# Kernel tuning notes

Measured on AMD Instinct MI355X. Metric: run time of the kernel, lower is better.

## Reference

```python
import jax, jax.numpy as jnp
import numpy as np
from jax import lax

NUM_SAMPLES = 16
EPSILON = 1e-08
CHUNK = 1024  # tile size for the reverse NN search (matches torch batch_size)


def _cdist(a, b):
    # Euclidean distance matrix [Na, Nb] via gemm form, numerically floored for sqrt.
    d2 = (a * a).sum(-1)[:, None] + (b * b).sum(-1)[None, :] - 2.0 * (a @ b.T)
    return jnp.sqrt(jnp.maximum(d2, 1e-12))


def setup_inputs() -> dict:
    key = jax.random.key(0)
    k = jax.random.split(key, 6)
    N, F, M, G = 16384, 16384, 4096, 8192
    return {
        "original_vertices": jax.random.normal(k[0], (N, 3), dtype=jnp.float32),
        "original_faces": jax.random.randint(k[1], (F, 3), 0, N),
        "simplified_vertices": jax.random.normal(k[2], (M, 3), dtype=jnp.float32),
        "simplified_faces": jax.random.randint(k[3], (G, 3), 0, M),
        "face_probabilities": jax.random.uniform(k[4], (G,), dtype=jnp.float32),
        "r1": jax.random.uniform(k[5], (G, NUM_SAMPLES, 1), dtype=jnp.float32),
        "r2": jax.random.uniform(jax.random.fold_in(key, 7), (G, NUM_SAMPLES, 1), dtype=jnp.float32),
    }


def reference(original_vertices, original_faces, simplified_vertices,
              simplified_faces, face_probabilities, r1, r2):
    G = simplified_faces.shape[0]
    probs = face_probabilities[:G]  # pad/slice to num simplified faces (identity here)

    # ---- forward term: simplified barycenters -> nearest original barycenter ----
    orig_bary = original_vertices[original_faces].mean(axis=1)      # [F,3]
    simp_bary = simplified_vertices[simplified_faces].mean(axis=1)  # [G,3]
    min_d = _cdist(simp_bary, orig_bary).min(axis=1)                # [G]
    forward_term = (probs * min_d).sum() + 1e-4 * (1.0 - probs).sum()

    # ---- reverse term: sample points on simplified faces, NN to original verts ----
    sqrt_r1 = jnp.sqrt(r1)
    u = 1.0 - sqrt_r1
    v = sqrt_r1 * (1.0 - r2)
    w = sqrt_r1 * r2
    fv = simplified_vertices[simplified_faces]  # [G,3,3]
    pts = (u * fv[:, None, 0] + v * fv[:, None, 1] + w * fv[:, None, 2]).reshape(-1, 3)

    total = pts.shape[0]  # G * NUM_SAMPLES, divisible by CHUNK
    vsq = (original_vertices * original_vertices).sum(-1)  # [N]

    def chunk_min(p):  # p: [CHUNK, 3]
        d2 = (p * p).sum(-1)[:, None] + vsq[None, :] - 2.0 * (p @ original_vertices.T)
        return jnp.sqrt(jnp.maximum(d2, 1e-12)).min(axis=1)

    mins = lax.map(chunk_min, pts.reshape(total // CHUNK, CHUNK, 3)).reshape(-1)
    max_dist = mins.max() + EPSILON
    scaled = mins / max_dist * 0.1
    probs_exp = jnp.repeat(probs, NUM_SAMPLES)
    reverse_term = (probs_exp * scaled).sum()

    return forward_term + reverse_term
```

## Files before the change

kernel.cpp:

```cpp
#include <hip/hip_runtime.h>
#include <math.h>

constexpr int N_V  = 16384;
constexpr int N_F  = 16384;
constexpr int G_F  = 8192;
constexpr int NS   = 16;
constexpr int NPTS = G_F * NS;

constexpr int MB    = 2;
constexpr int TILES = 32;

typedef _Float16 half8 __attribute__((ext_vector_type(8)));
typedef float    f32x16 __attribute__((ext_vector_type(16)));

constexpr int F4_ACC   = 0;
constexpr int F4_SB    = 1;
constexpr int F4_PTS   = F4_SB + G_F;
constexpr int F4_PKV   = F4_PTS + NPTS;
constexpr int F4_PKO   = F4_PKV + 32768;
constexpr int F4_TOTAL = F4_PKO + 32768;
constexpr int WS_MINF  = F4_TOTAL * 4;
constexpr int WS_MINR  = WS_MINF + G_F;

__device__ __forceinline__ void mfma4(half8 a0, half8 a1, half8 cA, half8 cB,
                                      f32x16& d0A, f32x16& d0B,
                                      f32x16& d1A, f32x16& d1B) {
  asm("v_mfma_f32_32x32x16_f16 %0, %4, %6, 0\n\t"
      "v_mfma_f32_32x32x16_f16 %1, %4, %7, 0\n\t"
      "v_mfma_f32_32x32x16_f16 %2, %5, %6, 0\n\t"
      "v_mfma_f32_32x32x16_f16 %3, %5, %7, 0\n\t"
      "s_nop 7\n\t"
      "s_nop 7\n\t"
      "s_nop 7\n\t"
      "s_nop 7\n\t"
      "s_nop 7\n\t"
      "s_nop 7"
      : "=&v"(d0A), "=&v"(d0B), "=&v"(d1A), "=&v"(d1B)
      : "v"(a0), "v"(a1), "v"(cA), "v"(cB));
}

__device__ __forceinline__ void pack_target(float x, float y, float z, float sq,
                                            half8* __restrict__ pk, int tile, int n) {
  float ax = -2.0f*x, ay = -2.0f*y, az = -2.0f*z;
  _Float16 hx = (_Float16)ax, hy = (_Float16)ay, hz = (_Float16)az, hw = (_Float16)sq;
  _Float16 lx = (_Float16)(ax - (float)hx), ly = (_Float16)(ay - (float)hy);
  _Float16 lz = (_Float16)(az - (float)hz), lw = (_Float16)(sq - (float)hw);
  half8 h0; h0[0]=hx; h0[1]=hy; h0[2]=hz; h0[3]=hw; h0[4]=lx; h0[5]=ly; h0[6]=lz; h0[7]=lw;
  half8 h1; h1[0]=hx; h1[1]=hy; h1[2]=hz; h1[3]=hw;
  h1[4]=(_Float16)0.0f; h1[5]=(_Float16)0.0f; h1[6]=(_Float16)0.0f; h1[7]=(_Float16)0.0f;
  pk[(size_t)tile*64 + n]      = h0;
  pk[(size_t)tile*64 + 32 + n] = h1;
}

__global__ void k_prep(const float* __restrict__ ov, const int* __restrict__ of,
                       const float* __restrict__ sv, const int* __restrict__ sf,
                       const float* __restrict__ r1, const float* __restrict__ r2,
                       unsigned int* __restrict__ ws, float4* __restrict__ ws4) {
  int i = blockIdx.x * blockDim.x + threadIdx.x;
  if (i < 4) ws[i] = 0u;
  ws[WS_MINR + i] = 0x7f800000u;

  {
    int g = i >> 4;
    int a = sf[3*g], b = sf[3*g+1], c = sf[3*g+2];
    float sr = sqrtf(r1[i]);
    float u = 1.0f - sr;
    float v = sr * (1.0f - r2[i]);
    float w = sr * r2[i];
    float px = u*sv[3*a]   + v*sv[3*b]   + w*sv[3*c];
    float py = u*sv[3*a+1] + v*sv[3*b+1] + w*sv[3*c+1];
    float pz = u*sv[3*a+2] + v*sv[3*b+2] + w*sv[3*c+2];
    (ws4 + F4_PTS)[i] = make_float4(px, py, pz, fmaf(px, px, fmaf(py, py, pz*pz)));
  }
  if (i < G_F) {
    ws[WS_MINF + i] = 0x7f800000u;
    int a = sf[3*i], b = sf[3*i+1], c = sf[3*i+2];
    float x = (sv[3*a] + sv[3*b] + sv[3*c]) * (1.0f/3.0f);
    float y = (sv[3*a+1] + sv[3*b+1] + sv[3*c+1]) * (1.0f/3.0f);
    float z = (sv[3*a+2] + sv[3*b+2] + sv[3*c+2]) * (1.0f/3.0f);
    (ws4 + F4_SB)[i] = make_float4(x, y, z, fmaf(x, x, fmaf(y, y, z*z)));
  }
  if (i < N_V) {
    float x = ov[3*i], y = ov[3*i+1], z = ov[3*i+2];
    pack_target(x, y, z, fmaf(x, x, fmaf(y, y, z*z)),
                (half8*)(ws4 + F4_PKV), i >> 5, i & 31);
  }
  if (i < N_F) {
    int a = of[3*i], b = of[3*i+1], c = of[3*i+2];
    float x = (ov[3*a] + ov[3*b] + ov[3*c]) * (1.0f/3.0f);
    float y = (ov[3*a+1] + ov[3*b+1] + ov[3*c+1]) * (1.0f/3.0f);
    float z = (ov[3*a+2] + ov[3*b+2] + ov[3*c+2]) * (1.0f/3.0f);
    pack_target(x, y, z, fmaf(x, x, fmaf(y, y, z*z)),
                (half8*)(ws4 + F4_PKO), i >> 5, i & 31);
  }
}

__global__ __launch_bounds__(256, 3) void k_min(const float4* __restrict__ q4,
                                                const half8* __restrict__ pk,
                                                unsigned int* __restrict__ minU,
                                                int nchunks) {
  __shared__ half8 sB[TILES * 64];
  int lane  = threadIdx.x & 63;
  int wave  = threadIdx.x >> 6;
  int half_ = lane >> 5;
  int m     = lane & 31;
  int qbase = blockIdx.x * 256 + wave * (32 * MB);
  int tbase = blockIdx.y * nchunks * TILES;

  half8 afrag[MB];
  float psq[MB];
  #pragma unroll
  for (int mb = 0; mb < MB; ++mb) {
    float4 q = q4[qbase + mb*32 + m];
    psq[mb] = q.w;
    _Float16 hx = (_Float16)q.x, hy = (_Float16)q.y, hz = (_Float16)q.z;
    half8 a;
    if (half_ == 0) {
      a[0]=hx; a[1]=hy; a[2]=hz; a[3]=(_Float16)1.0f;
      a[4]=hx; a[5]=hy; a[6]=hz; a[7]=(_Float16)1.0f;
    } else {
      a[0]=(_Float16)(q.x-(float)hx); a[1]=(_Float16)(q.y-(float)hy);
      a[2]=(_Float16)(q.z-(float)hz); a[3]=(_Float16)0.0f;
      a[4]=(_Float16)0.0f; a[5]=(_Float16)0.0f; a[6]=(_Float16)0.0f; a[7]=(_Float16)0.0f;
    }
    afrag[mb] = a;
  }

  float inf = __uint_as_float(0x7f800000u);
  float rm[MB][16];
  #pragma unroll
  for (int mb = 0; mb < MB; ++mb)
    #pragma unroll
    for (int r = 0; r < 16; ++r) rm[mb][r] = inf;

  for (int ch = 0; ch < nchunks; ++ch) {
    int t0 = tbase + ch * TILES;
    if (ch > 0) __syncthreads();
    const half8* src = pk + (size_t)(t0 + wave) * 64 + lane;
    #pragma unroll
    for (int j = 0; j < TILES/4; ++j) {
      __builtin_amdgcn_global_load_lds(
          (const __attribute__((address_space(1))) unsigned int*)(src + (size_t)j*256),
          (__attribute__((address_space(3))) unsigned int*)&sB[(wave + 4*j) * 64],
          16, 0, 0);
    }
    __syncthreads();

    for (int t = 0; t < TILES; t += 2) {
      half8 cA = sB[t*64 + lane];
      half8 cB = sB[t*64 + 64 + lane];
      f32x16 dA, dB, eA, eB;
      mfma4(afrag[0], afrag[1], cA, cB, dA, dB, eA, eB);
      #pragma unroll
      for (int r = 0; r < 16; ++r)
        rm[0][r] = fminf(fminf(rm[0][r], dA[r]), dB[r]);
      #pragma unroll
      for (int r = 0; r < 16; ++r)
        rm[1][r] = fminf(fminf(rm[1][r], eA[r]), eB[r]);
    }
  }

  #pragma unroll
  for (int mb = 0; mb < MB; ++mb) {
    #pragma unroll
    for (int r = 0; r < 16; ++r) {
      float v = rm[mb][r];
      v = fminf(v, __shfl_xor(v, 1, 64));
      v = fminf(v, __shfl_xor(v, 2, 64));
      v = fminf(v, __shfl_xor(v, 4, 64));
      v = fminf(v, __shfl_xor(v, 8, 64));
      v = fminf(v, __shfl_xor(v, 16, 64));
      int row = (r & 3) + 8*(r >> 2) + 4*half_;
      if (m == row) {
        float d2 = fmaxf(psq[mb] + v, 0.0f);
        atomicMin(&minU[qbase + mb*32 + m], __float_as_uint(d2));
      }
    }
  }
}

__device__ __forceinline__ float waveSum(float v) {
  #pragma unroll
  for (int o = 32; o > 0; o >>= 1) v += __shfl_down(v, o, 64);
  return v;
}
__device__ __forceinline__ float waveMax(float v) {
  #pragma unroll
  for (int o = 32; o > 0; o >>= 1) v = fmaxf(v, __shfl_down(v, o, 64));
  return v;
}

__global__ void k_reduce(const float* __restrict__ probs, const float* __restrict__ minf,
                         const float* __restrict__ minr, float* __restrict__ acc) {
  int tid = blockIdx.x * blockDim.x + threadIdx.x;
  int stride = gridDim.x * blockDim.x;
  float sf = 0.0f, sr = 0.0f, mx = 0.0f;
  for (int i = tid; i < NPTS; i += stride) {
    float d = sqrtf(fmaxf(minr[i], 1e-12f));
    sr = fmaf(probs[i >> 4], d, sr);
    mx = fmaxf(mx, d);
    if (i < G_F) {
      float df = sqrtf(fmaxf(minf[i], 1e-12f));
      sf = fmaf(probs[i], df, sf);
      sf = fmaf(1e-4f, 1.0f - probs[i], sf);
    }
  }
  __shared__ float lf[4], lr[4], lm[4];
  int lane = threadIdx.x & 63, wid = threadIdx.x >> 6;
  sf = waveSum(sf); sr = waveSum(sr); mx = waveMax(mx);
  if (lane == 0) { lf[wid] = sf; lr[wid] = sr; lm[wid] = mx; }
  __syncthreads();
  if (wid == 0) {
    float a = (lane < 4) ? lf[lane] : 0.0f;
    float b = (lane < 4) ? lr[lane] : 0.0f;
    float c = (lane < 4) ? lm[lane] : 0.0f;
    a = waveSum(a); b = waveSum(b); c = waveMax(c);
    if (lane == 0) {
      atomicAdd(&acc[0], a);
      atomicAdd(&acc[1], b);
      atomicMax((unsigned int*)&acc[2], __float_as_uint(c));
    }
  }
}

__global__ void k_final(const float* __restrict__ acc, float* __restrict__ out) {
  float maxd = acc[2] + 1e-8f;
  out[0] = acc[0] + acc[1] * 0.1f / maxd;
}

extern "C" void kernel_launch(void* const* d_in, const int* in_sizes, int n_in,
                              void* d_out, int out_size, void* d_ws, size_t ws_size,
                              hipStream_t stream) {
  const float* ov    = (const float*)d_in[0];
  const int*   of    = (const int*)  d_in[1];
  const float* sv    = (const float*)d_in[2];
  const int*   sfc   = (const int*)  d_in[3];
  const float* probs = (const float*)d_in[4];
  const float* r1    = (const float*)d_in[5];
  const float* r2    = (const float*)d_in[6];
  float*  ws  = (float*)d_ws;
  float4* ws4 = (float4*)d_ws;
  float*  out = (float*)d_out;

  float*        acc   = ws;
  float4*       sb4   = ws4 + F4_SB;
  float4*       pts4  = ws4 + F4_PTS;
  half8*        pkV   = (half8*)(ws4 + F4_PKV);
  half8*        pkO   = (half8*)(ws4 + F4_PKO);
  unsigned int* minfU = (unsigned int*)(ws + WS_MINF);
  unsigned int* minrU = (unsigned int*)(ws + WS_MINR);
  const float*  minfF = ws + WS_MINF;
  const float*  minrF = ws + WS_MINR;

  k_prep<<<NPTS/256, 256, 0, stream>>>(ov, of, sv, sfc, r1, r2,
                                       (unsigned int*)ws, ws4);
  k_min<<<dim3(G_F/256, 16), 256, 0, stream>>>(sb4, pkO, minfU, 1);
  k_min<<<dim3(NPTS/256, 8), 256, 0, stream>>>(pts4, pkV, minrU, 2);
  k_reduce<<<256, 256, 0, stream>>>(probs, minfF, minrF, acc);
  k_final<<<1, 1, 0, stream>>>(acc, out);
}
```

Baseline: 183.3 us.

## Fuse reverse-term reduction into NN kernel and software-pipeline MFMA min loop

The reverse nearest-neighbor kernel now runs over all 16384 target vertices per block (no y-split), so each query's minimum is final in-register. The sqrt, probability-weighted sum and max reduction happen there directly, replacing the per-point atomicMin buffer, its init, and the separate reduce kernel. Each wave handles one 32-query block instead of two. The MFMA loop is double-buffered so min reductions overlap the next MFMA pair, and occupancy hint rises to 4. The trade-off is less grid parallelism on the reverse pass and more per-wave serial work, with fewer launches and far less global memory traffic.

```diff
diff --git a/kernel.cpp b/kernel.cpp
--- a/kernel.cpp
+++ b/kernel.cpp
@@ -7,7 +7,6 @@
 constexpr int NS   = 16;
 constexpr int NPTS = G_F * NS;
 
-constexpr int MB    = 2;
 constexpr int TILES = 32;
 
 typedef _Float16 half8 __attribute__((ext_vector_type(8)));
@@ -20,23 +19,16 @@
 constexpr int F4_PKO   = F4_PKV + 32768;
 constexpr int F4_TOTAL = F4_PKO + 32768;
 constexpr int WS_MINF  = F4_TOTAL * 4;
-constexpr int WS_MINR  = WS_MINF + G_F;
-
-__device__ __forceinline__ void mfma4(half8 a0, half8 a1, half8 cA, half8 cB,
-                                      f32x16& d0A, f32x16& d0B,
-                                      f32x16& d1A, f32x16& d1B) {
-  asm("v_mfma_f32_32x32x16_f16 %0, %4, %6, 0\n\t"
-      "v_mfma_f32_32x32x16_f16 %1, %4, %7, 0\n\t"
-      "v_mfma_f32_32x32x16_f16 %2, %5, %6, 0\n\t"
-      "v_mfma_f32_32x32x16_f16 %3, %5, %7, 0\n\t"
-      "s_nop 7\n\t"
-      "s_nop 7\n\t"
-      "s_nop 7\n\t"
-      "s_nop 7\n\t"
-      "s_nop 7\n\t"
-      "s_nop 7"
-      : "=&v"(d0A), "=&v"(d0B), "=&v"(d1A), "=&v"(d1B)
-      : "v"(a0), "v"(a1), "v"(cA), "v"(cB));
+
+__device__ __forceinline__ void mfma2(half8 a, half8 cA, half8 cB,
+                                      f32x16& dA, f32x16& dB) {
+  asm volatile(
+      "v_mfma_f32_32x32x16_f16 %0, %2, %3, 0\n\t"
+      "v_mfma_f32_32x32x16_f16 %1, %2, %4, 0\n\t"
+      "s_nop 7\n\t" "s_nop 7\n\t" "s_nop 7\n\t"
+      "s_nop 7\n\t" "s_nop 7\n\t" "s_nop 7"
+      : "=&v"(dA), "=&v"(dB)
+      : "v"(a), "v"(cA), "v"(cB));
 }
 
 __device__ __forceinline__ void pack_target(float x, float y, float z, float sq,
@@ -58,7 +50,6 @@
                        unsigned int* __restrict__ ws, float4* __restrict__ ws4) {
   int i = blockIdx.x * blockDim.x + threadIdx.x;
   if (i < 4) ws[i] = 0u;
-  ws[WS_MINR + i] = 0x7f800000u;
 
   {
     int g = i >> 4;
@@ -95,43 +86,51 @@
   }
 }
 
-__global__ __launch_bounds__(256, 3) void k_min(const float4* __restrict__ q4,
+__device__ __forceinline__ float waveSum(float v) {
+  #pragma unroll
+  for (int o = 32; o > 0; o >>= 1) v += __shfl_down(v, o, 64);
+  return v;
+}
+__device__ __forceinline__ float waveMax(float v) {
+  #pragma unroll
+  for (int o = 32; o > 0; o >>= 1) v = fmaxf(v, __shfl_down(v, o, 64));
+  return v;
+}
+
+template <bool REV>
+__global__ __launch_bounds__(256, 4) void k_min(const float4* __restrict__ q4,
                                                 const half8* __restrict__ pk,
                                                 unsigned int* __restrict__ minU,
+                                                const float* __restrict__ probs,
+                                                float* __restrict__ acc,
                                                 int nchunks) {
   __shared__ half8 sB[TILES * 64];
   int lane  = threadIdx.x & 63;
   int wave  = threadIdx.x >> 6;
   int half_ = lane >> 5;
   int m     = lane & 31;
-  int qbase = blockIdx.x * 256 + wave * (32 * MB);
+  int qbase = blockIdx.x * 128 + wave * 32;
   int tbase = blockIdx.y * nchunks * TILES;
 
-  half8 afrag[MB];
-  float psq[MB];
-  #pragma unroll
-  for (int mb = 0; mb < MB; ++mb) {
-    float4 q = q4[qbase + mb*32 + m];
-    psq[mb] = q.w;
+  float4 q = q4[qbase + m];
+  float psq = q.w;
+  half8 af;
+  {
     _Float16 hx = (_Float16)q.x, hy = (_Float16)q.y, hz = (_Float16)q.z;
-    half8 a;
     if (half_ == 0) {
-      a[0]=hx; a[1]=hy; a[2]=hz; a[3]=(_Float16)1.0f;
-      a[4]=hx; a[5]=hy; a[6]=hz; a[7]=(_Float16)1.0f;
+      af[0]=hx; af[1]=hy; af[2]=hz; af[3]=(_Float16)1.0f;
+      af[4]=hx; af[5]=hy; af[6]=hz; af[7]=(_Float16)1.0f;
     } else {
-      a[0]=(_Float16)(q.x-(float)hx); a[1]=(_Float16)(q.y-(float)hy);
-      a[2]=(_Float16)(q.z-(float)hz); a[3]=(_Float16)0.0f;
-      a[4]=(_Float16)0.0f; a[5]=(_Float16)0.0f; a[6]=(_Float16)0.0f; a[7]=(_Float16)0.0f;
-    }
-    afrag[mb] = a;
+      af[0]=(_Float16)(q.x-(float)hx); af[1]=(_Float16)(q.y-(float)hy);
+      af[2]=(_Float16)(q.z-(float)hz); af[3]=(_Float16)0.0f;
+      af[4]=(_Float16)0.0f; af[5]=(_Float16)0.0f; af[6]=(_Float16)0.0f; af[7]=(_Float16)0.0f;
+    }
   }
 
   float inf = __uint_as_float(0x7f800000u);
-  float rm[MB][16];
-  #pragma unroll
-  for (int mb = 0; mb < MB; ++mb)
-    #pragma unroll
-    for (int r = 0; r < 16; ++r) rm[mb][r] = inf;
+  float rm[16];
+  #pragma unroll
+  for (int r = 0; r < 16; ++r) rm[r] = inf;
 
   for (int ch = 0; ch < nchunks; ++ch) {
     int t0 = tbase + ch * TILES;
@@ -146,86 +145,79 @@
     }
     __syncthreads();
 
-    for (int t = 0; t < TILES; t += 2) {
-      half8 cA = sB[t*64 + lane];
-      half8 cB = sB[t*64 + 64 + lane];
-      f32x16 dA, dB, eA, eB;
-      mfma4(afrag[0], afrag[1], cA, cB, dA, dB, eA, eB);
+    f32x16 d[2][2];
+    {
+      half8 cA = sB[lane];
+      half8 cB = sB[64 + lane];
+      mfma2(af, cA, cB, d[0][0], d[0][1]);
+    }
+    #pragma unroll
+    for (int p = 1; p < TILES/2; ++p) {
+      half8 nA = sB[(2*p)*64 + lane];
+      half8 nB = sB[(2*p)*64 + 64 + lane];
+      mfma2(af, nA, nB, d[p&1][0], d[p&1][1]);
+      int o = (p-1) & 1;
       #pragma unroll
       for (int r = 0; r < 16; ++r)
-        rm[0][r] = fminf(fminf(rm[0][r], dA[r]), dB[r]);
-      #pragma unroll
-      for (int r = 0; r < 16; ++r)
-        rm[1][r] = fminf(fminf(rm[1][r], eA[r]), eB[r]);
-    }
-  }
-
-  #pragma unroll
-  for (int mb = 0; mb < MB; ++mb) {
+        rm[r] = fminf(fminf(rm[r], d[o][0][r]), d[o][1][r]);
+    }
+    asm volatile("s_nop 7\n\ts_nop 7\n\ts_nop 7\n\ts_nop 7\n\ts_nop 7\n\ts_nop 7");
+    int o = (TILES/2 - 1) & 1;
     #pragma unroll
-    for (int r = 0; r < 16; ++r) {
-      float v = rm[mb][r];
-      v = fminf(v, __shfl_xor(v, 1, 64));
-      v = fminf(v, __shfl_xor(v, 2, 64));
-      v = fminf(v, __shfl_xor(v, 4, 64));
-      v = fminf(v, __shfl_xor(v, 8, 64));
-      v = fminf(v, __shfl_xor(v, 16, 64));
-      int row = (r & 3) + 8*(r >> 2) + 4*half_;
-      if (m == row) {
-        float d2 = fmaxf(psq[mb] + v, 0.0f);
-        atomicMin(&minU[qbase + mb*32 + m], __float_as_uint(d2));
+    for (int r = 0; r < 16; ++r)
+      rm[r] = fminf(fminf(rm[r], d[o][0][r]), d[o][1][r]);
+  }
+
+  float ps = 0.0f, pm = 0.0f;
+  #pragma unroll
+  for (int r = 0; r < 16; ++r) {
+    float v = rm[r];
+    v = fminf(v, __shfl_xor(v, 1, 64));
+    v = fminf(v, __shfl_xor(v, 2, 64));
+    v = fminf(v, __shfl_xor(v, 4, 64));
+    v = fminf(v, __shfl_xor(v, 8, 64));
+    v = fminf(v, __shfl_xor(v, 16, 64));
+    int row = (r & 3) + 8*(r >> 2) + 4*half_;
+    if (m == row) {
+      float d2 = fmaxf(psq + v, 0.0f);
+      if (REV) {
+        float dd = sqrtf(fmaxf(d2, 1e-12f));
+        ps = fmaf(probs[(qbase + row) >> 4], dd, ps);
+        pm = fmaxf(pm, dd);
+      } else {
+        atomicMin(&minU[qbase + row], __float_as_uint(d2));
       }
     }
   }
-}
-
-__device__ __forceinline__ float waveSum(float v) {
-  #pragma unroll
-  for (int o = 32; o > 0; o >>= 1) v += __shfl_down(v, o, 64);
-  return v;
-}
-__device__ __forceinline__ float waveMax(float v) {
-  #pragma unroll
-  for (int o = 32; o > 0; o >>= 1) v = fmaxf(v, __shfl_down(v, o, 64));
-  return v;
-}
-
-__global__ void k_reduce(const float* __restrict__ probs, const float* __restrict__ minf,
-                         const float* __restrict__ minr, float* __restrict__ acc) {
-  int tid = blockIdx.x * blockDim.x + threadIdx.x;
-  int stride = gridDim.x * blockDim.x;
-  float sf = 0.0f, sr = 0.0f, mx = 0.0f;
-  for (int i = tid; i < NPTS; i += stride) {
-    float d = sqrtf(fmaxf(minr[i], 1e-12f));
-    sr = fmaf(probs[i >> 4], d, sr);
-    mx = fmaxf(mx, d);
-    if (i < G_F) {
-      float df = sqrtf(fmaxf(minf[i], 1e-12f));
-      sf = fmaf(probs[i], df, sf);
-      sf = fmaf(1e-4f, 1.0f - probs[i], sf);
-    }
-  }
-  __shared__ float lf[4], lr[4], lm[4];
-  int lane = threadIdx.x & 63, wid = threadIdx.x >> 6;
-  sf = waveSum(sf); sr = waveSum(sr); mx = waveMax(mx);
-  if (lane == 0) { lf[wid] = sf; lr[wid] = sr; lm[wid] = mx; }
+  if (REV) {
+    ps = waveSum(ps);
+    pm = waveMax(pm);
+    if (lane == 0) {
+      atomicAdd(&acc[0], ps);
+      atomicMax((unsigned int*)&acc[1], __float_as_uint(pm));
+    }
+  }
+}
+
+__global__ void k_fin(const float* __restrict__ minf, const float* __restrict__ probs,
+                      const float* __restrict__ acc, float* __restrict__ out) {
+  int tid = threadIdx.x;
+  float sf = 0.0f;
+  for (int i = tid; i < G_F; i += 256) {
+    float df = sqrtf(fmaxf(minf[i], 1e-12f));
+    sf = fmaf(probs[i], df, sf);
+    sf = fmaf(1e-4f, 1.0f - probs[i], sf);
+  }
+  __shared__ float l[4];
+  int lane = tid & 63, wid = tid >> 6;
+  sf = waveSum(sf);
+  if (lane == 0) l[wid] = sf;
   __syncthreads();
-  if (wid == 0) {
-    float a = (lane < 4) ? lf[lane] : 0.0f;
-    float b = (lane < 4) ? lr[lane] : 0.0f;
-    float c = (lane < 4) ? lm[lane] : 0.0f;
-    a = waveSum(a); b = waveSum(b); c = waveMax(c);
-    if (lane == 0) {
-      atomicAdd(&acc[0], a);
-      atomicAdd(&acc[1], b);
-      atomicMax((unsigned int*)&acc[2], __float_as_uint(c));
-    }
-  }
-}
-
-__global__ void k_final(const float* __restrict__ acc, float* __restrict__ out) {
-  float maxd = acc[2] + 1e-8f;
-  out[0] = acc[0] + acc[1] * 0.1f / maxd;
+  if (tid == 0) {
+    float t = l[0] + l[1] + l[2] + l[3];
+    float maxd = acc[1] + 1e-8f;
+    out[0] = t + acc[0] * 0.1f / maxd;
+  }
 }
 
 extern "C" void kernel_launch(void* const* d_in, const int* in_sizes, int n_in,
@@ -248,14 +240,13 @@
   half8*        pkV   = (half8*)(ws4 + F4_PKV);
   half8*        pkO   = (half8*)(ws4 + F4_PKO);
   unsigned int* minfU = (unsigned int*)(ws + WS_MINF);
-  unsigned int* minrU = (unsigned int*)(ws + WS_MINR);
   const float*  minfF = ws + WS_MINF;
-  const float*  minrF = ws + WS_MINR;
 
   k_prep<<<NPTS/256, 256, 0, stream>>>(ov, of, sv, sfc, r1, r2,
                                        (unsigned int*)ws, ws4);
-  k_min<<<dim3(G_F/256, 16), 256, 0, stream>>>(sb4, pkO, minfU, 1);
-  k_min<<<dim3(NPTS/256, 8), 256, 0, stream>>>(pts4, pkV, minrU, 2);
-  k_reduce<<<256, 256, 0, stream>>>(probs, minfF, minrF, acc);
-  k_final<<<1, 1, 0, stream>>>(acc, out);
-}
+  k_min<false><<<dim3(G_F/128, 8), 256, 0, stream>>>(sb4, pkO, minfU,
+                                                     nullptr, nullptr, 2);
+  k_min<true><<<dim3(NPTS/128, 1), 256, 0, stream>>>(pts4, pkV, nullptr,
+                                                     probs, acc, 16);
+  k_fin<<<1, 256, 0, stream>>>(minfF, probs, acc, out);
+}
```

Measured after the change: 254.8 us. +39.0%, slower.
